# Kernel optimization log

Hardware: AMD Instinct MI355X
Metric: run time of the kernel (lower is better)

## Reference

```python
import jax, jax.numpy as jnp
import numpy as np

H = 128
NH = 8  # num attention heads


def _ln(x, g, b, eps=1e-5):
    m = x.mean(-1, keepdims=True)
    v = ((x - m) ** 2).mean(-1, keepdims=True)
    return (x - m) / jnp.sqrt(v + eps) * g + b


def _mha(q_in, kv_in, Wqkv, bqkv, Wo, bo):
    # torch nn.MultiheadAttention with packed in_proj, batch=1, eval (no dropout)
    h = q_in.shape[-1]
    hd = h // NH
    Wq, Wk, Wv = Wqkv[:h], Wqkv[h:2 * h], Wqkv[2 * h:]
    bq, bk, bv = bqkv[:h], bqkv[h:2 * h], bqkv[2 * h:]
    q = (q_in @ Wq.T + bq).reshape(-1, NH, hd).transpose(1, 0, 2)   # [nh, Nq, hd]
    k = (kv_in @ Wk.T + bk).reshape(-1, NH, hd).transpose(1, 0, 2)  # [nh, Nk, hd]
    v = (kv_in @ Wv.T + bv).reshape(-1, NH, hd).transpose(1, 0, 2)
    scores = jnp.einsum('hqd,hkd->hqk', q, k) / jnp.sqrt(jnp.asarray(hd, q.dtype))
    attn = jax.nn.softmax(scores, axis=-1)
    out = jnp.einsum('hqk,hkd->hqd', attn, v)                       # [nh, Nq, hd]
    out = out.transpose(1, 0, 2).reshape(-1, h)
    return out @ Wo.T + bo


def setup_inputs() -> dict:
    key = jax.random.key(0)
    ks = jax.random.split(key, 32)
    s = 0.05
    d = {
        'ligand_features': jax.random.normal(ks[0], (512, 128), jnp.float32),
        'pocket_features': jax.random.normal(ks[1], (1024, 128), jnp.float32),
        'ligand_coords': jax.random.uniform(ks[2], (512, 3), jnp.float32) * 20.0,
        'pocket_coords': jax.random.uniform(ks[3], (1024, 3), jnp.float32) * 20.0,
        # projections
        'Wl': jax.random.normal(ks[4], (H, 128), jnp.float32) * s,
        'bl': jnp.zeros((H,), jnp.float32),
        'Wp': jax.random.normal(ks[5], (H, 128), jnp.float32) * s,
        'bp': jnp.zeros((H,), jnp.float32),
        # distance encoder: 1 -> h/4 -> h/2 -> h
        'Wd1': jax.random.normal(ks[6], (H // 4, 1), jnp.float32) * s,
        'bd1': jnp.zeros((H // 4,), jnp.float32),
        'Wd2': jax.random.normal(ks[7], (H // 2, H // 4), jnp.float32) * s,
        'bd2': jnp.zeros((H // 2,), jnp.float32),
        'Wd3': jax.random.normal(ks[8], (H, H // 2), jnp.float32) * s,
        'bd3': jnp.zeros((H,), jnp.float32),
        # gates
        'Wgl': jax.random.normal(ks[9], (H, 2 * H), jnp.float32) * s,
        'bgl': jnp.zeros((H,), jnp.float32),
        'Wgp': jax.random.normal(ks[10], (H, 2 * H), jnp.float32) * s,
        'bgp': jnp.zeros((H,), jnp.float32),
        # shared cross-attention (packed qkv like torch)
        'Wqkv': jax.random.normal(ks[11], (3 * H, H), jnp.float32) * s,
        'bqkv': jnp.zeros((3 * H,), jnp.float32),
        'Wo': jax.random.normal(ks[12], (H, H), jnp.float32) * s,
        'bo': jnp.zeros((H,), jnp.float32),
        # layer norms
        'g_l': jnp.ones((H,), jnp.float32),
        'be_l': jnp.zeros((H,), jnp.float32),
        'g_p': jnp.ones((H,), jnp.float32),
        'be_p': jnp.zeros((H,), jnp.float32),
    }
    return d


def reference(ligand_features, pocket_features, ligand_coords, pocket_coords,
              Wl, bl, Wp, bp, Wd1, bd1, Wd2, bd2, Wd3, bd3,
              Wgl, bgl, Wgp, bgp, Wqkv, bqkv, Wo, bo,
              g_l, be_l, g_p, be_p):
    lig = ligand_features @ Wl.T + bl   # [Nl, H]
    poc = pocket_features @ Wp.T + bp   # [Np, H]

    # pairwise distances [Nl, Np]
    diff = ligand_coords[:, None, :] - pocket_coords[None, :, :]
    dist = jnp.sqrt(jnp.sum(diff * diff, axis=-1))

    # distance encoder MLP applied elementwise -> [Nl, Np, H]
    e = jax.nn.relu(dist[..., None] @ Wd1.T + bd1)
    e = jax.nn.relu(e @ Wd2.T + bd2)
    enc = e @ Wd3.T + bd3
    m = enc.mean(axis=-1)               # [Nl, Np]

    # ligand enhancement: softmax over pocket axis
    sw_l = jax.nn.softmax(-m, axis=-1)          # [Nl, Np]
    agg_l = sw_l @ poc                          # [Nl, H]
    gate_l = jax.nn.sigmoid(jnp.concatenate([lig, agg_l], axis=-1) @ Wgl.T + bgl)
    lig_enh = gate_l * lig + (1.0 - gate_l) * agg_l

    # pocket enhancement: transposed encoding, softmax over ligand axis
    sw_p = jax.nn.softmax(-m.T, axis=-1)        # [Np, Nl]
    agg_p = sw_p @ lig                          # [Np, H]
    gate_p = jax.nn.sigmoid(jnp.concatenate([poc, agg_p], axis=-1) @ Wgp.T + bgp)
    poc_enh = gate_p * poc + (1.0 - gate_p) * agg_p

    lig_att = _mha(lig_enh, poc_enh, Wqkv, bqkv, Wo, bo)
    poc_att = _mha(poc_enh, lig_enh, Wqkv, bqkv, Wo, bo)

    lig_fused = _ln(lig_enh + lig_att, g_l, be_l)
    poc_fused = _ln(poc_enh + poc_att, g_p, be_p)
    return (lig_fused, poc_fused)
```

## Files before the change

kernel.cpp:

```cpp
#include <hip/hip_runtime.h>
#include <math.h>

#define NL 512
#define NP 1024
#define HDIM 128

#define TAB_N 8192
#define DMAX 34.65f

#define M_OFF    128
#define WLT_OFF  (M_OFF)
#define WPT_OFF  (M_OFF + 16384)
#define WQT_OFF  (M_OFF + 32768)
#define WOT_OFF  (M_OFF + 81920)
#define WGLT_OFF (M_OFF + 98304)
#define WGPT_OFF (M_OFF + 131072)
#define TAB_OFF  (M_OFF + 163840)
#define LIG_OFF  (M_OFF + NL*NP)
#define POC_OFF  (LIG_OFF + NL*HDIM)
#define LENH_OFF (POC_OFF + NP*HDIM)
#define PENH_OFF (LENH_OFF + NL*HDIM)
#define QKVL_OFF (PENH_OFF + NP*HDIM)
#define QKVP_OFF (QKVL_OFF + NL*384)
#define PARTL_OFF (QKVP_OFF + NP*384)
#define PARTP_OFF (PARTL_OFF + 512*8*8*18)

__device__ __forceinline__ float dot4f(float4 a, float4 b){
  return fmaf(a.x,b.x, fmaf(a.y,b.y, fmaf(a.z,b.z, a.w*b.w)));
}

__device__ __forceinline__ void tpose(const float* __restrict__ src, float* __restrict__ dst,
                                      int O, int K, int blk0, int t){
  int e0 = blk0*1024 + t*4;
  #pragma unroll
  for (int i = 0; i < 4; i++){
    int e = e0 + i;
    int o = e / K, k = e - o*K;
    dst[(size_t)k*O + o] = src[(size_t)o*K + k];
  }
}
__global__ __launch_bounds__(256) void prep_all(const float* __restrict__ Wl, const float* __restrict__ Wp,
                                                const float* __restrict__ Wqkv, const float* __restrict__ Wo,
                                                const float* __restrict__ Wgl, const float* __restrict__ Wgp,
                                                const float* __restrict__ Wd1, const float* __restrict__ bd1,
                                                const float* __restrict__ Wd2, const float* __restrict__ bd2,
                                                const float* __restrict__ Wd3, const float* __restrict__ bd3,
                                                float* __restrict__ ws){
  int b = blockIdx.x, t = threadIdx.x;
  if (b < 160){
    if      (b < 16)  tpose(Wl,   ws + WLT_OFF,  128, 128, b,       t);
    else if (b < 32)  tpose(Wp,   ws + WPT_OFF,  128, 128, b - 16,  t);
    else if (b < 80)  tpose(Wqkv, ws + WQT_OFF,  384, 128, b - 32,  t);
    else if (b < 96)  tpose(Wo,   ws + WOT_OFF,  128, 128, b - 80,  t);
    else if (b < 128) tpose(Wgl,  ws + WGLT_OFF, 128, 256, b - 96,  t);
    else              tpose(Wgp,  ws + WGPT_OFF, 128, 256, b - 128, t);
    return;
  }
  float* tab = ws + TAB_OFF;
  __shared__ float sWd1[32], sbd1[32], sWd2[2048], sbd2[64], swd3m[64];
  __shared__ float sbd3m;
  int idx = (b - 160) * 256 + t;
  if (t < 64){
    float s = 0.f;
    #pragma unroll 8
    for (int i = 0; i < 128; i++) s += Wd3[i*64 + t];
    swd3m[t] = s * (1.f/128.f);
  } else if (t == 64){
    float s = 0.f;
    for (int i = 0; i < 128; i++) s += bd3[i];
    sbd3m = s * (1.f/128.f);
  } else if (t >= 128 && t < 160){ sWd1[t-128] = Wd1[t-128]; sbd1[t-128] = bd1[t-128]; }
  else if (t >= 160 && t < 224){ sbd2[t-160] = bd2[t-160]; }
  for (int k = t; k < 2048; k += 256) sWd2[k] = Wd2[k];
  __syncthreads();

  float d = (float)idx * (DMAX / (float)(TAB_N - 1));
  float4 e1q[8];
  const float4* w1q = (const float4*)sWd1;
  const float4* b1q = (const float4*)sbd1;
  #pragma unroll
  for (int k4 = 0; k4 < 8; k4++){
    float4 w = w1q[k4], bb = b1q[k4];
    float4 e;
    e.x = fmaxf(fmaf(d, w.x, bb.x), 0.f);
    e.y = fmaxf(fmaf(d, w.y, bb.y), 0.f);
    e.z = fmaxf(fmaf(d, w.z, bb.z), 0.f);
    e.w = fmaxf(fmaf(d, w.w, bb.w), 0.f);
    e1q[k4] = e;
  }
  float mv = sbd3m;
  #pragma unroll 4
  for (int j2 = 0; j2 < 64; j2++){
    const float4* wrow = (const float4*)(sWd2 + j2*32);
    float a0 = 0.f, a1 = 0.f, a2 = 0.f, a3 = 0.f;
    #pragma unroll
    for (int k4 = 0; k4 < 8; k4++){
      float4 w = wrow[k4], e = e1q[k4];
      a0 = fmaf(w.x, e.x, a0);
      a1 = fmaf(w.y, e.y, a1);
      a2 = fmaf(w.z, e.z, a2);
      a3 = fmaf(w.w, e.w, a3);
    }
    float e2v = fmaxf(sbd2[j2] + ((a0+a1)+(a2+a3)), 0.f);
    mv = fmaf(swd3m[j2], e2v, mv);
  }
  tab[idx] = mv;
}

__global__ __launch_bounds__(256) void proj_kernel(const float* __restrict__ lf, const float* __restrict__ pf,
                                                   const float* __restrict__ WlT, const float* __restrict__ bl,
                                                   const float* __restrict__ WpT, const float* __restrict__ bp,
                                                   float* __restrict__ lig, float* __restrict__ poc){
  int b = blockIdx.x, t = threadIdx.x;
  bool isLig = (b < NL/2);
  int r0 = isLig ? b*2 : (b - NL/2)*2;
  const float* in = (isLig ? lf : pf) + (size_t)r0*HDIM;
  const float* WT = isLig ? WlT : WpT;
  const float* bias = isLig ? bl : bp;
  float* out = (isLig ? lig : poc) + (size_t)r0*HDIM;
  __shared__ float sx[2*HDIM];
  sx[t] = in[t];
  __syncthreads();
  int r = t >> 7, col = t & 127;
  const float* xr = sx + r*HDIM;
  float acc = bias[col];
  #pragma unroll 8
  for (int k = 0; k < 128; k++) acc = fmaf(WT[k*128 + col], xr[k], acc);
  out[r*HDIM + col] = acc;
}

__global__ __launch_bounds__(512) void agg_gate_fused(const float* __restrict__ lc, const float* __restrict__ pc,
                                                      const float* __restrict__ tab,
                                                      const float* __restrict__ lig, const float* __restrict__ poc,
                                                      const float* __restrict__ WglT, const float* __restrict__ bgl,
                                                      const float* __restrict__ WgpT, const float* __restrict__ bgp,
                                                      const float* __restrict__ WqkvT, const float* __restrict__ bqkv,
                                                      float* __restrict__ lenh, float* __restrict__ penh,
                                                      float* __restrict__ qkvl, float* __restrict__ qkvp){
  int b = blockIdx.x, t = threadIdx.x;
  bool isLig = (b < NL/2);
  int r0 = isLig ? b*2 : (b - NL/2)*2;
  int n = isLig ? NP : NL;
  const float* myFeat = isLig ? lig : poc;
  const float* otherFeat = isLig ? poc : lig;
  const float* myC = isLig ? lc : pc;
  const float* otC = isLig ? pc : lc;

  __shared__ float w[2*NP];
  __shared__ float sx[2*HDIM];
  __shared__ float sa[2*HDIM];
  __shared__ float4 part4[8*64];
  __shared__ float gpart[512];
  __shared__ float redm[8];
  __shared__ float sgm[2], sinv[2];

  int rr = t >> 8, u = t & 255;
  int lane = t & 63, wv = t >> 6;
  int row = r0 + rr;

  if (t < 256) sx[t] = myFeat[(size_t)r0*HDIM + t];

// ... 92 lines not shown
    g = 1.0f / (1.0f + __expf(-g));
    float xv = sx[t], av = sa[t];
    enh_val = fmaf(g, xv - av, av);
    float* dst = isLig ? (lenh + (size_t)(r0+r)*HDIM) : (penh + (size_t)(r0+r)*HDIM);
    dst[col] = enh_val;
  }
  __syncthreads();
  if (t < 256) sa[t] = enh_val;
  __syncthreads();

  {
    int r = t >> 8, ln = t & 255;
    const float* er = sa + r*HDIM;
    float* qout = (isLig ? qkvl : qkvp) + (size_t)(r0+r)*384;
    if (ln < 128){
      float a0 = bqkv[ln], a2 = bqkv[ln+256];
      #pragma unroll 4
      for (int k = 0; k < 128; k++){
        float xv = er[k];
        const float* wk = WqkvT + k*384;
        a0 = fmaf(wk[ln],     xv, a0);
        a2 = fmaf(wk[ln+256], xv, a2);
      }
      qout[ln] = a0; qout[ln+256] = a2;
    } else {
      float a1 = bqkv[ln];
      #pragma unroll 4
      for (int k = 0; k < 128; k++) a1 = fmaf(WqkvT[k*384 + ln], er[k], a1);
      qout[ln] = a1;
    }
  }
}

__global__ __launch_bounds__(256) void attn_part(const float* __restrict__ qkvl, const float* __restrict__ qkvp,
                                                 float* __restrict__ partL, float* __restrict__ partP){
  int bx = blockIdx.x;
  int t = threadIdx.x;
  const float* qsrc; const float* kvsrc; int qt, slice; bool isLig;
  if (bx < 256){ isLig = true;  qt = bx >> 3; slice = bx & 7; qsrc = qkvl; kvsrc = qkvp; }
  else { int b2 = bx - 256; isLig = false; qt = b2 >> 2; slice = b2 & 3; qsrc = qkvp; kvsrc = qkvl; }
  int g = t >> 6, tt = t & 63;
  int h = tt >> 3, qp = tt & 7;
  int j0 = slice*128 + g*32;

  const float4* qA = (const float4*)(qsrc + (size_t)(qt*16+qp)*384 + h*16);
  const float4* qB = (const float4*)(qsrc + (size_t)(qt*16+qp+8)*384 + h*16);
  float4 a0 = qA[0], a1 = qA[1], a2 = qA[2], a3 = qA[3];
  float4 b0 = qB[0], b1 = qB[1], b2 = qB[2], b3 = qB[3];
  float mA = -1e30f, lA = 0.f, mB = -1e30f, lB = 0.f;
  float4 OA0={0,0,0,0}, OA1={0,0,0,0}, OA2={0,0,0,0}, OA3={0,0,0,0};
  float4 OB0={0,0,0,0}, OB1={0,0,0,0}, OB2={0,0,0,0}, OB3={0,0,0,0};

  __shared__ float sKV[8192];
  float* myKV = sKV + g*2048;

  for (int tile = 0; tile < 4; tile++){
    int jbase = j0 + tile*8;
    __syncthreads();
    #pragma unroll
    for (int nn = 0; nn < 8; nn++){
      int v4 = tt + nn*64;
      int jj = v4 >> 6, c4 = v4 & 63;
      ((float4*)myKV)[jj*64 + c4] = *(const float4*)(kvsrc + (size_t)(jbase+jj)*384 + 128 + c4*4);
    }
    __syncthreads();
    float sA[8], sB[8];
    #pragma unroll
    for (int jj = 0; jj < 8; jj++){
      const float4* kk = (const float4*)(myKV + jj*256 + h*16);
      float4 k0 = kk[0], k1 = kk[1], k2 = kk[2], k3 = kk[3];
      sA[jj] = (dot4f(a0,k0) + dot4f(a1,k1) + dot4f(a2,k2) + dot4f(a3,k3)) * 0.25f;
      sB[jj] = (dot4f(b0,k0) + dot4f(b1,k1) + dot4f(b2,k2) + dot4f(b3,k3)) * 0.25f;
    }
    float mtA = sA[0], mtB = sB[0];
    #pragma unroll
    for (int jj = 1; jj < 8; jj++){ mtA = fmaxf(mtA, sA[jj]); mtB = fmaxf(mtB, sB[jj]); }
    float mnA = fmaxf(mA, mtA), mnB = fmaxf(mB, mtB);
    float cA = __expf(mA - mnA), cB = __expf(mB - mnB);
    lA *= cA; lB *= cB;
    OA0.x*=cA; OA0.y*=cA; OA0.z*=cA; OA0.w*=cA;
    OA1.x*=cA; OA1.y*=cA; OA1.z*=cA; OA1.w*=cA;
    OA2.x*=cA; OA2.y*=cA; OA2.z*=cA; OA2.w*=cA;
    OA3.x*=cA; OA3.y*=cA; OA3.z*=cA; OA3.w*=cA;
    OB0.x*=cB; OB0.y*=cB; OB0.z*=cB; OB0.w*=cB;
    OB1.x*=cB; OB1.y*=cB; OB1.z*=cB; OB1.w*=cB;
    OB2.x*=cB; OB2.y*=cB; OB2.z*=cB; OB2.w*=cB;
// ... 53 lines not shown
      float e0 = __expf(M - Mn), e1 = __expf(m1 - Mn);
      L = L*e0 + l1*e1;
      #pragma unroll
      for (int k = 0; k < 16; k++) O[k] = O[k]*e0 + br[2+k]*e1;
      M = Mn;
    }
    int rowA = qt*16 + qp;
    float* dst = isLig ? (partL + ((size_t)(rowA*8 + h)*8 + slice)*18)
                       : (partP + ((size_t)(rowA*8 + h)*4 + slice)*18);
    dst[0] = M; dst[1] = L;
    #pragma unroll
    for (int k = 0; k < 16; k++) dst[2+k] = O[k];
    M = mB; L = lB;
    float Ob[16] = {OB0.x,OB0.y,OB0.z,OB0.w, OB1.x,OB1.y,OB1.z,OB1.w,
                    OB2.x,OB2.y,OB2.z,OB2.w, OB3.x,OB3.y,OB3.z,OB3.w};
    #pragma unroll
    for (int gg = 1; gg < 4; gg++){
      const float* br = sKV + (size_t)((gg-1)*128 + tt*2 + 1)*19;
      float m1 = br[0], l1 = br[1];
      float Mn = fmaxf(M, m1);
      float e0 = __expf(M - Mn), e1 = __expf(m1 - Mn);
      L = L*e0 + l1*e1;
      #pragma unroll
      for (int k = 0; k < 16; k++) Ob[k] = Ob[k]*e0 + br[2+k]*e1;
      M = Mn;
    }
    int rowB = qt*16 + qp + 8;
    float* dstB = isLig ? (partL + ((size_t)(rowB*8 + h)*8 + slice)*18)
                        : (partP + ((size_t)(rowB*8 + h)*4 + slice)*18);
    dstB[0] = M; dstB[1] = L;
    #pragma unroll
    for (int k = 0; k < 16; k++) dstB[2+k] = Ob[k];
  }
}

__global__ __launch_bounds__(256) void merge_ln(const float* __restrict__ partL, const float* __restrict__ partP,
                                                const float* __restrict__ lenh, const float* __restrict__ penh,
                                                const float* __restrict__ WoT, const float* __restrict__ bo,
                                                const float* __restrict__ g_l, const float* __restrict__ be_l,
                                                const float* __restrict__ g_p, const float* __restrict__ be_p,
                                                float* __restrict__ out){
  int b = blockIdx.x, t = threadIdx.x;
  int r0 = b*2;
  int r = t >> 7, c = t & 127;
  int gr = r0 + r;
  int h = c >> 4, cc = c & 15;
  int ns; const float* base;
  if (gr < NL){ ns = 8; base = partL + ((size_t)(gr*8 + h))*8*18; }
  else        { ns = 4; base = partP + ((size_t)((gr-NL)*8 + h))*4*18; }
  float M = -1e30f;
  for (int s = 0; s < ns; s++) M = fmaxf(M, base[s*18]);
  float Lsum = 0.f, Osum = 0.f;
  for (int s = 0; s < ns; s++){
    float e = __expf(base[s*18] - M);
    Lsum = fmaf(e, base[s*18+1], Lsum);
    Osum = fmaf(e, base[s*18+2+cc], Osum);
  }
  __shared__ float sAtt[2*HDIM];
  sAtt[t] = Osum / Lsum;
  __syncthreads();
  float o = bo[c];
  const float* sA = sAtt + r*HDIM;
  #pragma unroll 8
  for (int k = 0; k < 128; k++) o = fmaf(WoT[k*128 + c], sA[k], o);
  const float* enh = (gr < NL) ? (lenh + (size_t)gr*HDIM) : (penh + (size_t)(gr-NL)*HDIM);
  float x = enh[c] + o;
  __shared__ float sred[8];
  int wid = t >> 6;
  float v = x;
  #pragma unroll
  for (int off = 32; off; off >>= 1) v += __shfl_down(v, off);
  if ((t & 63) == 0) sred[wid] = v;
  __syncthreads();
  float mu = (sred[2*r] + sred[2*r+1]) * (1.f/128.f);
  float dx = x - mu;
  v = dx*dx;
  #pragma unroll
  for (int off = 32; off; off >>= 1) v += __shfl_down(v, off);
  if ((t & 63) == 0) sred[4 + wid] = v;
  __syncthreads();
  float var = (sred[4 + 2*r] + sred[4 + 2*r+1]) * (1.f/128.f);
  float y = dx * rsqrtf(var + 1e-5f);
  if (gr < NL) y = fmaf(y, g_l[c], be_l[c]);
  else         y = fmaf(y, g_p[c], be_p[c]);
  out[(size_t)gr*HDIM + c] = y;
}

extern "C" void kernel_launch(void* const* d_in, const int* in_sizes, int n_in,
                              void* d_out, int out_size, void* d_ws, size_t ws_size,
                              hipStream_t stream){
  const float* lf   = (const float*)d_in[0];
  const float* pf   = (const float*)d_in[1];
  const float* lc   = (const float*)d_in[2];
  const float* pc   = (const float*)d_in[3];
  const float* Wl   = (const float*)d_in[4];
  const float* bl   = (const float*)d_in[5];
  const float* Wp   = (const float*)d_in[6];
  const float* bp   = (const float*)d_in[7];
  const float* Wd1  = (const float*)d_in[8];
  const float* bd1  = (const float*)d_in[9];
  const float* Wd2  = (const float*)d_in[10];
  const float* bd2  = (const float*)d_in[11];
  const float* Wd3  = (const float*)d_in[12];
  const float* bd3  = (const float*)d_in[13];
  const float* Wgl  = (const float*)d_in[14];
  const float* bgl  = (const float*)d_in[15];
  const float* Wgp  = (const float*)d_in[16];
  const float* bgp  = (const float*)d_in[17];
  const float* Wqkv = (const float*)d_in[18];
  const float* bqkv = (const float*)d_in[19];
  const float* Wo   = (const float*)d_in[20];
  const float* bo   = (const float*)d_in[21];
  const float* g_l  = (const float*)d_in[22];
  const float* be_l = (const float*)d_in[23];
  const float* g_p  = (const float*)d_in[24];
  const float* be_p = (const float*)d_in[25];

  float* ws  = (float*)d_ws;
  float* out = (float*)d_out;
  float* lig   = ws + LIG_OFF;
  float* poc   = ws + POC_OFF;
  float* lenh  = ws + LENH_OFF;
  float* penh  = ws + PENH_OFF;
  float* qkvl  = ws + QKVL_OFF;
  float* qkvp  = ws + QKVP_OFF;
  float* partL = ws + PARTL_OFF;
  float* partP = ws + PARTP_OFF;
  float* tab   = ws + TAB_OFF;

  prep_all<<<192, 256, 0, stream>>>(Wl, Wp, Wqkv, Wo, Wgl, Wgp, Wd1, bd1, Wd2, bd2, Wd3, bd3, ws);
  proj_kernel<<<NL/2 + NP/2, 256, 0, stream>>>(lf, pf, ws + WLT_OFF, bl, ws + WPT_OFF, bp, lig, poc);
  agg_gate_fused<<<NL/2 + NP/2, 512, 0, stream>>>(lc, pc, tab, lig, poc,
                                                  ws + WGLT_OFF, bgl, ws + WGPT_OFF, bgp,
                                                  ws + WQT_OFF, bqkv,
                                                  lenh, penh, qkvl, qkvp);
  attn_part<<<512, 256, 0, stream>>>(qkvl, qkvp, partL, partP);
  merge_ln<<<NL/2 + NP/2, 256, 0, stream>>>(partL, partP, lenh, penh, ws + WOT_OFF, bo,
                                            g_l, be_l, g_p, be_p, out);
}
```

Measured before the change: 194.5 us.

## Fuse all stages into one cooperative persistent kernel with grid syncs

```diff
diff --git a/kernel.cpp b/kernel.cpp
--- a/kernel.cpp
+++ b/kernel.cpp
@@ -1,5 +1,8 @@
 #include <hip/hip_runtime.h>
+#include <hip/hip_cooperative_groups.h>
 #include <math.h>
+
+namespace cg = cooperative_groups;
 
 #define NL 512
 #define NP 1024
@@ -24,9 +27,487 @@
 #define QKVP_OFF (QKVL_OFF + NL*384)
 #define PARTL_OFF (QKVP_OFF + NP*384)
 #define PARTP_OFF (PARTL_OFF + 512*8*8*18)
+#define AGG_OFF   (PARTP_OFF + 1024*8*4*18)
 
 __device__ __forceinline__ float dot4f(float4 a, float4 b){
   return fmaf(a.x,b.x, fmaf(a.y,b.y, fmaf(a.z,b.z, a.w*b.w)));
+}
+
+__global__ __launch_bounds__(512, 4) void fused_all(
+  const float* __restrict__ lf, const float* __restrict__ pf,
+  const float* __restrict__ lc, const float* __restrict__ pc,
+  const float* __restrict__ Wl, const float* __restrict__ bl,
+  const float* __restrict__ Wp, const float* __restrict__ bp,
+  const float* __restrict__ Wd1, const float* __restrict__ bd1,
+  const float* __restrict__ Wd2, const float* __restrict__ bd2,
+  const float* __restrict__ Wd3, const float* __restrict__ bd3,
+  const float* __restrict__ Wgl, const float* __restrict__ bgl,
+  const float* __restrict__ Wgp, const float* __restrict__ bgp,
+  const float* __restrict__ Wqkv, const float* __restrict__ bqkv,
+  const float* __restrict__ Wo, const float* __restrict__ bo,
+  const float* __restrict__ g_l, const float* __restrict__ be_l,
+  const float* __restrict__ g_p, const float* __restrict__ be_p,
+  float* __restrict__ ws, float* __restrict__ out)
+{
+  cg::grid_group grd = cg::this_grid();
+  const int b = blockIdx.x;
+  const int t = threadIdx.x;
+
+  __shared__ __align__(16) float smem[16384];
+
+  float* WlT   = ws + WLT_OFF;
+  float* WpT   = ws + WPT_OFF;
+  float* WqkvT = ws + WQT_OFF;
+  float* WoT   = ws + WOT_OFF;
+  float* WglT  = ws + WGLT_OFF;
+  float* WgpT  = ws + WGPT_OFF;
+  float* tab   = ws + TAB_OFF;
+  float* lig   = ws + LIG_OFF;
+  float* poc   = ws + POC_OFF;
+  float* lenh  = ws + LENH_OFF;
+  float* penh  = ws + PENH_OFF;
+  float* qkvl  = ws + QKVL_OFF;
+  float* qkvp  = ws + QKVP_OFF;
+  float* partL = ws + PARTL_OFF;
+  float* partP = ws + PARTP_OFF;
+  float* aggb  = ws + AGG_OFF;
+
+  {
+    int e = b*512 + t;
+    if (e < 163840){
+      if (e < 16384){
+        int loc = e, o = loc >> 7, k = loc & 127;
+        WlT[k*128 + o] = Wl[loc];
+      } else if (e < 32768){
+        int loc = e - 16384, o = loc >> 7, k = loc & 127;
+        WpT[k*128 + o] = Wp[loc];
+      } else if (e < 81920){
+        int loc = e - 32768, o = loc >> 7, k = loc & 127;
+        WqkvT[k*384 + o] = Wqkv[loc];
+      } else if (e < 98304){
+        int loc = e - 81920, o = loc >> 7, k = loc & 127;
+        WoT[k*128 + o] = Wo[loc];
+      } else if (e < 131072){
+        int loc = e - 98304, o = loc >> 8, k = loc & 255;
+        WglT[k*128 + o] = Wgl[loc];
+      } else {
+        int loc = e - 131072, o = loc >> 8, k = loc & 255;
+        WgpT[k*128 + o] = Wgp[loc];
+      }
+    }
+  }
+  grd.sync();
+
+  if (b < 384){
+    int sub = t >> 8, st = t & 255;
+    int s = b*2 + sub;
+    bool isLig = (s < NL/2);
+    int r0 = isLig ? s*2 : (s - NL/2)*2;
+    const float* in  = (isLig ? lf : pf) + (size_t)r0*HDIM;
+    const float* WT  = isLig ? WlT : WpT;
+    const float* bia = isLig ? bl : bp;
+    float* o = (isLig ? lig : poc) + (size_t)r0*HDIM;
+    float* sx = smem + sub*256;
+    sx[st] = in[st];
+    __syncthreads();
+    int r = st >> 7, col = st & 127;
+    const float* xr = sx + r*HDIM;
+    float acc = bia[col];
+    #pragma unroll 8
+    for (int k = 0; k < 128; k++) acc = fmaf(WT[k*128 + col], xr[k], acc);
+    o[r*HDIM + col] = acc;
+  } else if (b < 400){
+    float* sWd1  = smem;
+    float* sbd1  = smem + 32;
+    float* sbd2  = smem + 64;
+    float* swd3m = smem + 128;
+    float* sWd2  = smem + 256;
+    if (t < 64){
+      float ssum = 0.f;
+      #pragma unroll 8
+      for (int i = 0; i < 128; i++) ssum += Wd3[i*64 + t];
+      swd3m[t] = ssum * (1.f/128.f);
+    } else if (t == 64){
+      float ssum = 0.f;
+      for (int i = 0; i < 128; i++) ssum += bd3[i];
+      smem[192] = ssum * (1.f/128.f);
+    } else if (t >= 128 && t < 160){ sWd1[t-128] = Wd1[t-128]; sbd1[t-128] = bd1[t-128]; }
+    else if (t >= 160 && t < 224){ sbd2[t-160] = bd2[t-160]; }
+    for (int k = t; k < 2048; k += 512) sWd2[k] = Wd2[k];
+    __syncthreads();
+
+    int idx = (b - 384)*512 + t;
+    float d = (float)idx * (DMAX / (float)(TAB_N - 1));
+    float4 e1q[8];
+    const float4* w1q = (const float4*)sWd1;
+    const float4* b1q = (const float4*)sbd1;
+    #pragma unroll
+    for (int k4 = 0; k4 < 8; k4++){
+      float4 w = w1q[k4], bb = b1q[k4];
+      float4 e;
+      e.x = fmaxf(fmaf(d, w.x, bb.x), 0.f);
+      e.y = fmaxf(fmaf(d, w.y, bb.y), 0.f);
+      e.z = fmaxf(fmaf(d, w.z, bb.z), 0.f);
+      e.w = fmaxf(fmaf(d, w.w, bb.w), 0.f);
+      e1q[k4] = e;
+    }
+    float mv = smem[192];
+    #pragma unroll 4
+    for (int j2 = 0; j2 < 64; j2++){
+      const float4* wrow = (const float4*)(sWd2 + j2*32);
+      float a0 = 0.f, a1 = 0.f, a2 = 0.f, a3 = 0.f;
+      #pragma unroll
+      for (int k4 = 0; k4 < 8; k4++){
+        float4 w = wrow[k4], e = e1q[k4];
+        a0 = fmaf(w.x, e.x, a0);
+        a1 = fmaf(w.y, e.y, a1);
+        a2 = fmaf(w.z, e.z, a2);
+        a3 = fmaf(w.w, e.w, a3);
+      }
+      float e2v = fmaxf(sbd2[j2] + ((a0+a1)+(a2+a3)), 0.f);
+      mv = fmaf(swd3m[j2], e2v, mv);
+    }
+    tab[idx] = mv;
+  }
+  grd.sync();
+
+  {
+    float*  w     = smem;
+    float4* part4 = (float4*)(smem + 2048);
+    float*  redm  = smem + 4096;
+    float*  sgm   = smem + 4104;
+    float*  sinv  = smem + 4106;
+
+    int ntask = (b < 256) ? 1 : 2;
+    bool isLig = (b < 256);
+    int n = isLig ? NP : NL;
+    const float* otherFeat = isLig ? poc : lig;
+    const float* myC = isLig ? lc : pc;
+    const float* otC = isLig ? pc : lc;
+    int growbase = isLig ? 0 : NL;
+    const float inv_h = (float)(TAB_N - 1) / DMAX;
+
+    int rr = t >> 8, u = t & 255;
+    int lane = t & 63, wv = t >> 6;
+    int per = n >> 8;
+
+    for (int it = 0; it < ntask; it++){
+      int r0 = isLig ? b*2 : (2*(b-256) + it)*2;
+      int row = r0 + rr;
+      float cx = myC[row*3+0], cy = myC[row*3+1], cz = myC[row*3+2];
+
+      float xs[4];
+      float lmax = -1e30f;
+      for (int k = 0; k < per; k++){
+        int j = u + (k << 8);
+        float ox = otC[j*3+0], oy = otC[j*3+1], oz = otC[j*3+2];
+        float dx = cx-ox, dy = cy-oy, dz = cz-oz;
+        float d = sqrtf(fmaf(dx,dx, fmaf(dy,dy, dz*dz)));
+        float xf = d * inv_h;
+        int i0 = (int)xf;
+        i0 = (i0 > TAB_N-2) ? (TAB_N-2) : i0;
+        float f = xf - (float)i0;
+        float v0 = tab[i0], v1 = tab[i0+1];
+        xs[k] = -fmaf(f, v1 - v0, v0);
+        lmax = fmaxf(lmax, xs[k]);
+      }
+      float v = lmax;
+      #pragma unroll
+      for (int off = 32; off; off >>= 1) v = fmaxf(v, __shfl_down(v, off));
+      if (lane == 0) redm[wv] = v;
+      __syncthreads();
+      if (t < 2) sgm[t] = fmaxf(fmaxf(redm[t*4+0], redm[t*4+1]), fmaxf(redm[t*4+2], redm[t*4+3]));
+      __syncthreads();
+      float gm = sgm[rr];
+      float lsum = 0.f;
+      for (int k = 0; k < per; k++){
+        float e = __expf(xs[k] - gm);
+        w[rr*NP + u + (k << 8)] = e;
+        lsum += e;
+      }
+      v = lsum;
+      #pragma unroll
+      for (int off = 32; off; off >>= 1) v += __shfl_down(v, off);
+      if (lane == 0) redm[wv] = v;
+      __syncthreads();
+      if (t < 2) sinv[t] = 1.0f / ((redm[t*4+0] + redm[t*4+1]) + (redm[t*4+2] + redm[t*4+3]));
+      __syncthreads();
+
+      {
+        int jg = t >> 6;
+        int r  = (t >> 5) & 1;
+        int c4 = t & 31;
+        int per2 = n >> 3;
+        int jb0 = jg * per2;
+        const float4* of4 = (const float4*)otherFeat;
+        const float* wR = w + r*NP;
+        float4 acc = {0,0,0,0};
+        #pragma unroll 4
+        for (int jj = 0; jj < per2; jj++){
+          int j = jb0 + jj;
+          float4 f = of4[(size_t)j*32 + c4];
+          float ww = wR[j];
+          acc.x = fmaf(ww, f.x, acc.x); acc.y = fmaf(ww, f.y, acc.y);
+          acc.z = fmaf(ww, f.z, acc.z); acc.w = fmaf(ww, f.w, acc.w);
+        }
+        part4[(jg*2 + r)*32 + c4] = acc;
+      }
+      __syncthreads();
+      #pragma unroll
+      for (int s2 = 4; s2 >= 1; s2 >>= 1){
+        if (t < s2*64){
+          int g2 = t >> 6, rem = t & 63;
+          float4 a = part4[g2*64 + rem], bb = part4[(g2+s2)*64 + rem];
+          a.x += bb.x; a.y += bb.y; a.z += bb.z; a.w += bb.w;
+          part4[g2*64 + rem] = a;
+        }
+        __syncthreads();
+      }
+      if (t < 256){
+        float val = ((const float*)part4)[t] * sinv[t >> 7];
+        aggb[(size_t)(growbase + r0 + (t >> 7))*HDIM + (t & 127)] = val;
+      }
+      __syncthreads();
+    }
+  }
+  grd.sync();
+
+  {
+    float* sx    = smem;
+    float* sa2   = smem + 128;
+    float* se    = smem + 256;
+    float* gpart = smem + 384;
+    for (int i = 0; i < 3; i++){
+      int grow = b + i*512;
+      bool isLig = (grow < NL);
+      int row = isLig ? grow : grow - NL;
+      const float* xsrc = (isLig ? lig : poc) + (size_t)row*HDIM;
+      if (t < 128){ sx[t] = xsrc[t]; sa2[t] = aggb[(size_t)grow*HDIM + t]; }
+      __syncthreads();
+      {
+        int col = t & 127, kg = t >> 7;
+        const float* WT = isLig ? WglT : WgpT;
+        const float* inb = (kg < 2) ? sx : (sa2 - 128);
+        int k0 = kg*64;
+        float acc = 0.f;
+        #pragma unroll 8
+        for (int kk = 0; kk < 64; kk++){
+          int k = k0 + kk;
+          acc = fmaf(WT[(size_t)k*128 + col], inb[k], acc);
+        }
+        gpart[kg*128 + col] = acc;
+      }
+      __syncthreads();
+      if (t < 128){
+        const float* bg = isLig ? bgl : bgp;
+        float g = bg[t] + ((gpart[t] + gpart[128+t]) + (gpart[256+t] + gpart[384+t]));
+        g = 1.0f / (1.0f + __expf(-g));
+        float xv = sx[t], av = sa2[t];
+        float enh = fmaf(g, xv - av, av);
+        se[t] = enh;
+        float* dst = isLig ? (lenh + (size_t)row*HDIM) : (penh + (size_t)row*HDIM);
+        dst[t] = enh;
+      }
+      __syncthreads();
+      if (t < 384){
+        float acc = bqkv[t];
+        #pragma unroll 8
+        for (int k = 0; k < 128; k++) acc = fmaf(WqkvT[(size_t)k*384 + t], se[k], acc);
+        float* q = (isLig ? qkvl : qkvp) + (size_t)row*384;
+        q[t] = acc;
+      }
+      __syncthreads();
+    }
+  }
+  grd.sync();
+
+  {
+    const float* qsrc; const float* kvsrc; int qt, slice; bool isLig;
+    if (b < 256){ isLig = true;  qt = b >> 3; slice = b & 7; qsrc = qkvl; kvsrc = qkvp; }
+    else { int b2 = b - 256; isLig = false; qt = b2 >> 2; slice = b2 & 3; qsrc = qkvp; kvsrc = qkvl; }
+    int g = t >> 6, tt = t & 63;
+    int h = tt >> 3, qp = tt & 7;
+    int j0 = slice*128 + g*16;
+
+    const float4* qA = (const float4*)(qsrc + (size_t)(qt*16+qp)*384 + h*16);
+    const float4* qB = (const float4*)(qsrc + (size_t)(qt*16+qp+8)*384 + h*16);
+    float4 a0 = qA[0], a1 = qA[1], a2 = qA[2], a3 = qA[3];
+    float4 b0 = qB[0], b1 = qB[1], b2 = qB[2], b3 = qB[3];
+    float mA = -1e30f, lA = 0.f, mB = -1e30f, lB = 0.f;
+    float4 OA0={0,0,0,0}, OA1={0,0,0,0}, OA2={0,0,0,0}, OA3={0,0,0,0};
+    float4 OB0={0,0,0,0}, OB1={0,0,0,0}, OB2={0,0,0,0}, OB3={0,0,0,0};
+
+    float* myKV = smem + g*2048;
+
+    for (int tile = 0; tile < 2; tile++){
+      int jbase = j0 + tile*8;
+      __syncthreads();
+      #pragma unroll
+      for (int nn = 0; nn < 8; nn++){
+        int v4 = tt + nn*64;
+        int jj = v4 >> 6, c4 = v4 & 63;
+        ((float4*)myKV)[jj*64 + c4] = *(const float4*)(kvsrc + (size_t)(jbase+jj)*384 + 128 + c4*4);
+      }
+      __syncthreads();
+      float sA[8], sB[8];
+      #pragma unroll
+      for (int jj = 0; jj < 8; jj++){
+        const float4* kk = (const float4*)(myKV + jj*256 + h*16);
+        float4 k0 = kk[0], k1 = kk[1], k2 = kk[2], k3 = kk[3];
+        sA[jj] = (dot4f(a0,k0) + dot4f(a1,k1) + dot4f(a2,k2) + dot4f(a3,k3)) * 0.25f;
+        sB[jj] = (dot4f(b0,k0) + dot4f(b1,k1) + dot4f(b2,k2) + dot4f(b3,k3)) * 0.25f;
+      }
+      float mtA = sA[0], mtB = sB[0];
+      #pragma unroll
+      for (int jj = 1; jj < 8; jj++){ mtA = fmaxf(mtA, sA[jj]); mtB = fmaxf(mtB, sB[jj]); }
+      float mnA = fmaxf(mA, mtA), mnB = fmaxf(mB, mtB);
+      float cA = __expf(mA - mnA), cB = __expf(mB - mnB);
+      lA *= cA; lB *= cB;
+      OA0.x*=cA; OA0.y*=cA; OA0.z*=cA; OA0.w*=cA;
+      OA1.x*=cA; OA1.y*=cA; OA1.z*=cA; OA1.w*=cA;
+      OA2.x*=cA; OA2.y*=cA; OA2.z*=cA; OA2.w*=cA;
+      OA3.x*=cA; OA3.y*=cA; OA3.z*=cA; OA3.w*=cA;
+      OB0.x*=cB; OB0.y*=cB; OB0.z*=cB; OB0.w*=cB;
+      OB1.x*=cB; OB1.y*=cB; OB1.z*=cB; OB1.w*=cB;
+      OB2.x*=cB; OB2.y*=cB; OB2.z*=cB; OB2.w*=cB;
+      OB3.x*=cB; OB3.y*=cB; OB3.z*=cB; OB3.w*=cB;
+      #pragma unroll
+      for (int jj = 0; jj < 8; jj++){
+        float pA = __expf(sA[jj] - mnA);
+        float pB = __expf(sB[jj] - mnB);
+        lA += pA; lB += pB;
+        const float4* vv = (const float4*)(myKV + jj*256 + 128 + h*16);
+        float4 v0 = vv[0], v1 = vv[1], v2 = vv[2], v3 = vv[3];
+        OA0.x = fmaf(pA, v0.x, OA0.x); OA0.y = fmaf(pA, v0.y, OA0.y);
+        OA0.z = fmaf(pA, v0.z, OA0.z); OA0.w = fmaf(pA, v0.w, OA0.w);
+        OA1.x = fmaf(pA, v1.x, OA1.x); OA1.y = fmaf(pA, v1.y, OA1.y);
+        OA1.z = fmaf(pA, v1.z, OA1.z); OA1.w = fmaf(pA, v1.w, OA1.w);
+        OA2.x = fmaf(pA, v2.x, OA2.x); OA2.y = fmaf(pA, v2.y, OA2.y);
+        OA2.z = fmaf(pA, v2.z, OA2.z); OA2.w = fmaf(pA, v2.w, OA2.w);
+        OA3.x = fmaf(pA, v3.x, OA3.x); OA3.y = fmaf(pA, v3.y, OA3.y);
+        OA3.z = fmaf(pA, v3.z, OA3.z); OA3.w = fmaf(pA, v3.w, OA3.w);
+        OB0.x = fmaf(pB, v0.x, OB0.x); OB0.y = fmaf(pB, v0.y, OB0.y);
+        OB0.z = fmaf(pB, v0.z, OB0.z); OB0.w = fmaf(pB, v0.w, OB0.w);
+        OB1.x = fmaf(pB, v1.x, OB1.x); OB1.y = fmaf(pB, v1.y, OB1.y);
+        OB1.z = fmaf(pB, v1.z, OB1.z); OB1.w = fmaf(pB, v1.w, OB1.w);
+        OB2.x = fmaf(pB, v2.x, OB2.x); OB2.y = fmaf(pB, v2.y, OB2.y);
+        OB2.z = fmaf(pB, v2.z, OB2.z); OB2.w = fmaf(pB, v2.w, OB2.w);
+        OB3.x = fmaf(pB, v3.x, OB3.x); OB3.y = fmaf(pB, v3.y, OB3.y);
+        OB3.z = fmaf(pB, v3.z, OB3.z); OB3.w = fmaf(pB, v3.w, OB3.w);
+      }
+      mA = mnA; mB = mnB;
+    }
+
+    __syncthreads();
+    if (g > 0){
+      float* bA = smem + (size_t)((g-1)*128 + tt*2)*18;
+      bA[0]=mA; bA[1]=lA;
+      bA[2]=OA0.x; bA[3]=OA0.y; bA[4]=OA0.z; bA[5]=OA0.w;
+      bA[6]=OA1.x; bA[7]=OA1.y; bA[8]=OA1.z; bA[9]=OA1.w;
+      bA[10]=OA2.x; bA[11]=OA2.y; bA[12]=OA2.z; bA[13]=OA2.w;
+      bA[14]=OA3.x; bA[15]=OA3.y; bA[16]=OA3.z; bA[17]=OA3.w;
+      float* bB = bA + 18;
+      bB[0]=mB; bB[1]=lB;
+      bB[2]=OB0.x; bB[3]=OB0.y; bB[4]=OB0.z; bB[5]=OB0.w;
+      bB[6]=OB1.x; bB[7]=OB1.y; bB[8]=OB1.z; bB[9]=OB1.w;
+      bB[10]=OB2.x; bB[11]=OB2.y; bB[12]=OB2.z; bB[13]=OB2.w;
+      bB[14]=OB3.x; bB[15]=OB3.y; bB[16]=OB3.z; bB[17]=OB3.w;
+    }
+    __syncthreads();
+    if (g == 0){
+      float M = mA, L = lA;
+      float O[16] = {OA0.x,OA0.y,OA0.z,OA0.w, OA1.x,OA1.y,OA1.z,OA1.w,
+                     OA2.x,OA2.y,OA2.z,OA2.w, OA3.x,OA3.y,OA3.z,OA3.w};
+      #pragma unroll
+      for (int gg = 1; gg < 8; gg++){
+        const float* br = smem + (size_t)((gg-1)*128 + tt*2)*18;
+        float m1 = br[0], l1 = br[1];
+        float Mn = fmaxf(M, m1);
+        float e0 = __expf(M - Mn), e1 = __expf(m1 - Mn);
+        L = L*e0 + l1*e1;
+        #pragma unroll
+        for (int k = 0; k < 16; k++) O[k] = O[k]*e0 + br[2+k]*e1;
+        M = Mn;
+      }
+      int rowA = qt*16 + qp;
+      float* dst = isLig ? (partL + ((size_t)(rowA*8 + h)*8 + slice)*18)
+                         : (partP + ((size_t)(rowA*8 + h)*4 + slice)*18);
+      dst[0] = M; dst[1] = L;
+      #pragma unroll
+      for (int k = 0; k < 16; k++) dst[2+k] = O[k];
+      M = mB; L = lB;
+      float Ob[16] = {OB0.x,OB0.y,OB0.z,OB0.w, OB1.x,OB1.y,OB1.z,OB1.w,
+                      OB2.x,OB2.y,OB2.z,OB2.w, OB3.x,OB3.y,OB3.z,OB3.w};
+      #pragma unroll
+      for (int gg = 1; gg < 8; gg++){
+        const float* br = smem + (size_t)((gg-1)*128 + tt*2)*18 + 18;
+        float m1 = br[0], l1 = br[1];
+        float Mn = fmaxf(M, m1);
+        float e0 = __expf(M - Mn), e1 = __expf(m1 - Mn);
+        L = L*e0 + l1*e1;
+        #pragma unroll
+        for (int k = 0; k < 16; k++) Ob[k] = Ob[k]*e0 + br[2+k]*e1;
+        M = Mn;
+      }
+      int rowB = qt*16 + qp + 8;
+      float* dstB = isLig ? (partL + ((size_t)(rowB*8 + h)*8 + slice)*18)
+                          : (partP + ((size_t)(rowB*8 + h)*4 + slice)*18);
+      dstB[0] = M; dstB[1] = L;
+      #pragma unroll
+      for (int k = 0; k < 16; k++) dstB[2+k] = Ob[k];
+    }
+  }
+  grd.sync();
+
+  {
+    int sub = t >> 8, st = t & 255;
+    int s = b*2 + sub;
+    if (s < 768){
+      int r0 = s*2;
+      int r = st >> 7, c = st & 127;
+      int gr = r0 + r;
+      int hh = c >> 4, cc = c & 15;
+      int ns; const float* base;
+      if (gr < NL){ ns = 8; base = partL + ((size_t)(gr*8 + hh))*8*18; }
+      else        { ns = 4; base = partP + ((size_t)((gr-NL)*8 + hh))*4*18; }
+      float M = -1e30f;
+      for (int sl = 0; sl < ns; sl++) M = fmaxf(M, base[sl*18]);
+      float Lsum = 0.f, Osum = 0.f;
+      for (int sl = 0; sl < ns; sl++){
+        float e = __expf(base[sl*18] - M);
+        Lsum = fmaf(e, base[sl*18+1], Lsum);
+        Osum = fmaf(e, base[sl*18+2+cc], Osum);
+      }
+      float* sAtt = smem + sub*512;
+      float* sred = smem + 1024 + sub*16;
+      sAtt[st] = Osum / Lsum;
+      __syncthreads();
+      float o = bo[c];
+      const float* sA = sAtt + r*HDIM;
+      #pragma unroll 8
+      for (int k = 0; k < 128; k++) o = fmaf(WoT[k*128 + c], sA[k], o);
+      const float* enh = (gr < NL) ? (lenh + (size_t)gr*HDIM) : (penh + (size_t)(gr-NL)*HDIM);
+      float x = enh[c] + o;
+      int wid = st >> 6;
+      float v = x;
+      #pragma unroll
+      for (int off = 32; off; off >>= 1) v += __shfl_down(v, off);
+      if ((st & 63) == 0) sred[wid] = v;
+      __syncthreads();
+      float mu = (sred[2*r] + sred[2*r+1]) * (1.f/128.f);
+      float dx = x - mu;
+      v = dx*dx;
+      #pragma unroll
+      for (int off = 32; off; off >>= 1) v += __shfl_down(v, off);
+      if ((st & 63) == 0) sred[4 + wid] = v;
+      __syncthreads();
+      float var = (sred[4 + 2*r] + sred[4 + 2*r+1]) * (1.f/128.f);
+      float y = dx * rsqrtf(var + 1e-5f);
+      if (gr < NL) y = fmaf(y, g_l[c], be_l[c]);
+      else         y = fmaf(y, g_p[c], be_p[c]);
+      out[(size_t)gr*HDIM + c] = y;
+    }
+  }
 }
 
 __device__ __forceinline__ void tpose(const float* __restrict__ src, float* __restrict__ dst,
@@ -510,23 +991,36 @@
 
   float* ws  = (float*)d_ws;
   float* out = (float*)d_out;
-  float* lig   = ws + LIG_OFF;
-  float* poc   = ws + POC_OFF;
-  float* lenh  = ws + LENH_OFF;
-  float* penh  = ws + PENH_OFF;
-  float* qkvl  = ws + QKVL_OFF;
-  float* qkvp  = ws + QKVP_OFF;
-  float* partL = ws + PARTL_OFF;
-  float* partP = ws + PARTP_OFF;
-  float* tab   = ws + TAB_OFF;
-
-  prep_all<<<192, 256, 0, stream>>>(Wl, Wp, Wqkv, Wo, Wgl, Wgp, Wd1, bd1, Wd2, bd2, Wd3, bd3, ws);
-  proj_kernel<<<NL/2 + NP/2, 256, 0, stream>>>(lf, pf, ws + WLT_OFF, bl, ws + WPT_OFF, bp, lig, poc);
-  agg_gate_fused<<<NL/2 + NP/2, 512, 0, stream>>>(lc, pc, tab, lig, poc,
-                                                  ws + WGLT_OFF, bgl, ws + WGPT_OFF, bgp,
-                                                  ws + WQT_OFF, bqkv,
-                                                  lenh, penh, qkvl, qkvp);
-  attn_part<<<512, 256, 0, stream>>>(qkvl, qkvp, partL, partP);
-  merge_ln<<<NL/2 + NP/2, 256, 0, stream>>>(partL, partP, lenh, penh, ws + WOT_OFF, bo,
-                                            g_l, be_l, g_p, be_p, out);
+
+  void* args[] = { (void*)&lf, (void*)&pf, (void*)&lc, (void*)&pc,
+                   (void*)&Wl, (void*)&bl, (void*)&Wp, (void*)&bp,
+                   (void*)&Wd1, (void*)&bd1, (void*)&Wd2, (void*)&bd2,
+                   (void*)&Wd3, (void*)&bd3, (void*)&Wgl, (void*)&bgl,
+                   (void*)&Wgp, (void*)&bgp, (void*)&Wqkv, (void*)&bqkv,
+                   (void*)&Wo, (void*)&bo, (void*)&g_l, (void*)&be_l,
+                   (void*)&g_p, (void*)&be_p, (void*)&ws, (void*)&out };
+
+  hipError_t err = hipLaunchCooperativeKernel((const void*)fused_all,
+                                              dim3(512), dim3(512), args, 0, stream);
+  if (err != hipSuccess){
+    float* lig   = ws + LIG_OFF;
+    float* poc   = ws + POC_OFF;
+    float* lenh  = ws + LENH_OFF;
+    float* penh  = ws + PENH_OFF;
+    float* qkvl  = ws + QKVL_OFF;
+    float* qkvp  = ws + QKVP_OFF;
+    float* partL = ws + PARTL_OFF;
+    float* partP = ws + PARTP_OFF;
+    float* tab   = ws + TAB_OFF;
+
+    prep_all<<<192, 256, 0, stream>>>(Wl, Wp, Wqkv, Wo, Wgl, Wgp, Wd1, bd1, Wd2, bd2, Wd3, bd3, ws);
+    proj_kernel<<<NL/2 + NP/2, 256, 0, stream>>>(lf, pf, ws + WLT_OFF, bl, ws + WPT_OFF, bp, lig, poc);
+    agg_gate_fused<<<NL/2 + NP/2, 512, 0, stream>>>(lc, pc, tab, lig, poc,
+                                                    ws + WGLT_OFF, bgl, ws + WGPT_OFF, bgp,
+                                                    ws + WQT_OFF, bqkv,
+                                                    lenh, penh, qkvl, qkvp);
+    attn_part<<<512, 256, 0, stream>>>(qkvl, qkvp, partL, partP);
+    merge_ln<<<NL/2 + NP/2, 256, 0, stream>>>(partL, partP, lenh, penh, ws + WOT_OFF, bo,
+                                              g_l, be_l, g_p, be_p, out);
+  }
 }
```

New measurement: 565.9 us. 191% more time.

## Fuse input projection into prep kernel and merge+LN into attention via last-block counter

Applied to the files above, without the earlier changes.

```diff
diff --git a/kernel.cpp b/kernel.cpp
--- a/kernel.cpp
+++ b/kernel.cpp
@@ -9,14 +9,12 @@
 #define DMAX 34.65f
 
 #define M_OFF    128
-#define WLT_OFF  (M_OFF)
-#define WPT_OFF  (M_OFF + 16384)
-#define WQT_OFF  (M_OFF + 32768)
-#define WOT_OFF  (M_OFF + 81920)
-#define WGLT_OFF (M_OFF + 98304)
-#define WGPT_OFF (M_OFF + 131072)
-#define TAB_OFF  (M_OFF + 163840)
-#define LIG_OFF  (M_OFF + NL*NP)
+#define WQT_OFF  (M_OFF)
+#define WOT_OFF  (M_OFF + 49152)
+#define WGLT_OFF (M_OFF + 65536)
+#define WGPT_OFF (M_OFF + 98304)
+#define TAB_OFF  (M_OFF + 131072)
+#define LIG_OFF  (M_OFF + 139264)
 #define POC_OFF  (LIG_OFF + NL*HDIM)
 #define LENH_OFF (POC_OFF + NP*HDIM)
 #define PENH_OFF (LENH_OFF + NL*HDIM)
@@ -24,6 +22,7 @@
 #define QKVP_OFF (QKVL_OFF + NL*384)
 #define PARTL_OFF (QKVP_OFF + NP*384)
 #define PARTP_OFF (PARTL_OFF + 512*8*8*18)
+#define CNT_OFF   (PARTP_OFF + 1024*8*4*18)
 
 __device__ __forceinline__ float dot4f(float4 a, float4 b){
   return fmaf(a.x,b.x, fmaf(a.y,b.y, fmaf(a.z,b.z, a.w*b.w)));
@@ -39,27 +38,54 @@
     dst[(size_t)k*O + o] = src[(size_t)o*K + k];
   }
 }
-__global__ __launch_bounds__(256) void prep_all(const float* __restrict__ Wl, const float* __restrict__ Wp,
-                                                const float* __restrict__ Wqkv, const float* __restrict__ Wo,
-                                                const float* __restrict__ Wgl, const float* __restrict__ Wgp,
-                                                const float* __restrict__ Wd1, const float* __restrict__ bd1,
-                                                const float* __restrict__ Wd2, const float* __restrict__ bd2,
-                                                const float* __restrict__ Wd3, const float* __restrict__ bd3,
-                                                float* __restrict__ ws){
+
+__global__ __launch_bounds__(256) void prep_proj(
+    const float* __restrict__ lf, const float* __restrict__ pf,
+    const float* __restrict__ Wl, const float* __restrict__ bl,
+    const float* __restrict__ Wp, const float* __restrict__ bp,
+    const float* __restrict__ Wqkv, const float* __restrict__ Wo,
+    const float* __restrict__ Wgl, const float* __restrict__ Wgp,
+    const float* __restrict__ Wd1, const float* __restrict__ bd1,
+    const float* __restrict__ Wd2, const float* __restrict__ bd2,
+    const float* __restrict__ Wd3, const float* __restrict__ bd3,
+    float* __restrict__ ws){
   int b = blockIdx.x, t = threadIdx.x;
-  if (b < 160){
-    if      (b < 16)  tpose(Wl,   ws + WLT_OFF,  128, 128, b,       t);
-    else if (b < 32)  tpose(Wp,   ws + WPT_OFF,  128, 128, b - 16,  t);
-    else if (b < 80)  tpose(Wqkv, ws + WQT_OFF,  384, 128, b - 32,  t);
-    else if (b < 96)  tpose(Wo,   ws + WOT_OFF,  128, 128, b - 80,  t);
-    else if (b < 128) tpose(Wgl,  ws + WGLT_OFF, 128, 256, b - 96,  t);
-    else              tpose(Wgp,  ws + WGPT_OFF, 128, 256, b - 128, t);
+
+  if (b < 768){
+    bool isLig = (b < 256);
+    int r0 = isLig ? b*2 : (b - 256)*2;
+    const float* in   = (isLig ? lf : pf) + (size_t)r0*HDIM;
+    const float* W    = isLig ? Wl : Wp;
+    const float* bias = isLig ? bl : bp;
+    float* out = ws + (isLig ? LIG_OFF : POC_OFF) + (size_t)r0*HDIM;
+    __shared__ __align__(16) float sx[2*HDIM];
+    sx[t] = in[t];
+    __syncthreads();
+    int r = t >> 7, col = t & 127;
+    const float4* xr4 = (const float4*)(sx + r*HDIM);
+    const float4* w4  = (const float4*)(W + (size_t)col*128);
+    float acc = bias[col];
+    #pragma unroll 8
+    for (int k4 = 0; k4 < 32; k4++) acc += dot4f(w4[k4], xr4[k4]);
+    out[r*HDIM + col] = acc;
     return;
   }
+
+  if (b < 896){
+    int bb = b - 768;
+    if      (bb < 48) tpose(Wqkv, ws + WQT_OFF,  384, 128, bb,      t);
+    else if (bb < 64) tpose(Wo,   ws + WOT_OFF,  128, 128, bb - 48, t);
+    else if (bb < 96) tpose(Wgl,  ws + WGLT_OFF, 128, 256, bb - 64, t);
+    else              tpose(Wgp,  ws + WGPT_OFF, 128, 256, bb - 96, t);
+    return;
+  }
+
+  if (b == 896 && t < 96) ((int*)(ws + CNT_OFF))[t] = 0;
+
   float* tab = ws + TAB_OFF;
   __shared__ float sWd1[32], sbd1[32], sWd2[2048], sbd2[64], swd3m[64];
   __shared__ float sbd3m;
-  int idx = (b - 160) * 256 + t;
+  int idx = (b - 896) * 256 + t;
   if (t < 64){
     float s = 0.f;
     #pragma unroll 8
@@ -80,12 +106,12 @@
   const float4* b1q = (const float4*)sbd1;
   #pragma unroll
   for (int k4 = 0; k4 < 8; k4++){
-    float4 w = w1q[k4], bb = b1q[k4];
+    float4 w = w1q[k4], bb2 = b1q[k4];
     float4 e;
-    e.x = fmaxf(fmaf(d, w.x, bb.x), 0.f);
-    e.y = fmaxf(fmaf(d, w.y, bb.y), 0.f);
-    e.z = fmaxf(fmaf(d, w.z, bb.z), 0.f);
-    e.w = fmaxf(fmaf(d, w.w, bb.w), 0.f);
+    e.x = fmaxf(fmaf(d, w.x, bb2.x), 0.f);
+    e.y = fmaxf(fmaf(d, w.y, bb2.y), 0.f);
+    e.z = fmaxf(fmaf(d, w.z, bb2.z), 0.f);
+    e.w = fmaxf(fmaf(d, w.w, bb2.w), 0.f);
     e1q[k4] = e;
   }
   float mv = sbd3m;
@@ -105,28 +131,6 @@
     mv = fmaf(swd3m[j2], e2v, mv);
   }
   tab[idx] = mv;
-}
-
-__global__ __launch_bounds__(256) void proj_kernel(const float* __restrict__ lf, const float* __restrict__ pf,
-                                                   const float* __restrict__ WlT, const float* __restrict__ bl,
-                                                   const float* __restrict__ WpT, const float* __restrict__ bp,
-                                                   float* __restrict__ lig, float* __restrict__ poc){
-  int b = blockIdx.x, t = threadIdx.x;
-  bool isLig = (b < NL/2);
-  int r0 = isLig ? b*2 : (b - NL/2)*2;
-  const float* in = (isLig ? lf : pf) + (size_t)r0*HDIM;
-  const float* WT = isLig ? WlT : WpT;
-  const float* bias = isLig ? bl : bp;
-  float* out = (isLig ? lig : poc) + (size_t)r0*HDIM;
-  __shared__ float sx[2*HDIM];
-  sx[t] = in[t];
-  __syncthreads();
-  int r = t >> 7, col = t & 127;
-  const float* xr = sx + r*HDIM;
-  float acc = bias[col];
-  #pragma unroll 8
-  for (int k = 0; k < 128; k++) acc = fmaf(WT[k*128 + col], xr[k], acc);
-  out[r*HDIM + col] = acc;
 }
 
 __global__ __launch_bounds__(512) void agg_gate_fused(const float* __restrict__ lc, const float* __restrict__ pc,
@@ -285,8 +289,13 @@
   }
 }
 
-__global__ __launch_bounds__(256) void attn_part(const float* __restrict__ qkvl, const float* __restrict__ qkvp,
-                                                 float* __restrict__ partL, float* __restrict__ partP){
+__global__ __launch_bounds__(256) void attn_merge(const float* __restrict__ qkvl, const float* __restrict__ qkvp,
+                                                  float* __restrict__ partL, float* __restrict__ partP,
+                                                  const float* __restrict__ lenh, const float* __restrict__ penh,
+                                                  const float* __restrict__ WoT, const float* __restrict__ bo,
+                                                  const float* __restrict__ g_l, const float* __restrict__ be_l,
+                                                  const float* __restrict__ g_p, const float* __restrict__ be_p,
+                                                  int* __restrict__ cnt, float* __restrict__ out){
   int bx = blockIdx.x;
   int t = threadIdx.x;
   const float* qsrc; const float* kvsrc; int qt, slice; bool isLig;
@@ -304,7 +313,7 @@
   float4 OA0={0,0,0,0}, OA1={0,0,0,0}, OA2={0,0,0,0}, OA3={0,0,0,0};
   float4 OB0={0,0,0,0}, OB1={0,0,0,0}, OB2={0,0,0,0}, OB3={0,0,0,0};
 
-  __shared__ float sKV[8192];
+  __shared__ __align__(16) float sKV[8192];
   float* myKV = sKV + g*2048;
 
   for (int tile = 0; tile < 4; tile++){
@@ -424,58 +433,66 @@
     #pragma unroll
     for (int k = 0; k < 16; k++) dstB[2+k] = Ob[k];
   }
-}
-
-__global__ __launch_bounds__(256) void merge_ln(const float* __restrict__ partL, const float* __restrict__ partP,
-                                                const float* __restrict__ lenh, const float* __restrict__ penh,
-                                                const float* __restrict__ WoT, const float* __restrict__ bo,
-                                                const float* __restrict__ g_l, const float* __restrict__ be_l,
-                                                const float* __restrict__ g_p, const float* __restrict__ be_p,
-                                                float* __restrict__ out){
-  int b = blockIdx.x, t = threadIdx.x;
-  int r0 = b*2;
+
+  __syncthreads();
+  __threadfence();
+  __shared__ int sWin;
+  if (t == 0){
+    int idx = isLig ? qt : (32 + qt);
+    int target = isLig ? 8 : 4;
+    int old = atomicAdd(&cnt[idx], 1);
+    sWin = (old == target - 1) ? 1 : 0;
+  }
+  __syncthreads();
+  if (!sWin) return;
+  __threadfence();
+
+  float* sAtt = sKV;
+  float* sred = sKV + 512;
   int r = t >> 7, c = t & 127;
-  int gr = r0 + r;
-  int h = c >> 4, cc = c & 15;
-  int ns; const float* base;
-  if (gr < NL){ ns = 8; base = partL + ((size_t)(gr*8 + h))*8*18; }
-  else        { ns = 4; base = partP + ((size_t)((gr-NL)*8 + h))*4*18; }
-  float M = -1e30f;
-  for (int s = 0; s < ns; s++) M = fmaxf(M, base[s*18]);
-  float Lsum = 0.f, Osum = 0.f;
-  for (int s = 0; s < ns; s++){
-    float e = __expf(base[s*18] - M);
-    Lsum = fmaf(e, base[s*18+1], Lsum);
-    Osum = fmaf(e, base[s*18+2+cc], Osum);
-  }
-  __shared__ float sAtt[2*HDIM];
-  sAtt[t] = Osum / Lsum;
-  __syncthreads();
-  float o = bo[c];
-  const float* sA = sAtt + r*HDIM;
-  #pragma unroll 8
-  for (int k = 0; k < 128; k++) o = fmaf(WoT[k*128 + c], sA[k], o);
-  const float* enh = (gr < NL) ? (lenh + (size_t)gr*HDIM) : (penh + (size_t)(gr-NL)*HDIM);
-  float x = enh[c] + o;
-  __shared__ float sred[8];
+  int hh = c >> 4, cc = c & 15;
   int wid = t >> 6;
-  float v = x;
-  #pragma unroll
-  for (int off = 32; off; off >>= 1) v += __shfl_down(v, off);
-  if ((t & 63) == 0) sred[wid] = v;
-  __syncthreads();
-  float mu = (sred[2*r] + sred[2*r+1]) * (1.f/128.f);
-  float dx = x - mu;
-  v = dx*dx;
-  #pragma unroll
-  for (int off = 32; off; off >>= 1) v += __shfl_down(v, off);
-  if ((t & 63) == 0) sred[4 + wid] = v;
-  __syncthreads();
-  float var = (sred[4 + 2*r] + sred[4 + 2*r+1]) * (1.f/128.f);
-  float y = dx * rsqrtf(var + 1e-5f);
-  if (gr < NL) y = fmaf(y, g_l[c], be_l[c]);
-  else         y = fmaf(y, g_p[c], be_p[c]);
-  out[(size_t)gr*HDIM + c] = y;
+  for (int i = 0; i < 8; i++){
+    int lr = qt*16 + 2*i + r;
+    int ns; const float* base;
+    if (isLig){ ns = 8; base = partL + ((size_t)(lr*8 + hh))*8*18; }
+    else      { ns = 4; base = partP + ((size_t)(lr*8 + hh))*4*18; }
+    float M = -1e30f;
+    for (int sl = 0; sl < ns; sl++) M = fmaxf(M, base[sl*18]);
+    float Lsum = 0.f, Osum = 0.f;
+    for (int sl = 0; sl < ns; sl++){
+      float e = __expf(base[sl*18] - M);
+      Lsum = fmaf(e, base[sl*18+1], Lsum);
+      Osum = fmaf(e, base[sl*18+2+cc], Osum);
+    }
+    __syncthreads();
+    sAtt[t] = Osum / Lsum;
+    __syncthreads();
+    float o = bo[c];
+    const float* sA = sAtt + r*HDIM;
+    #pragma unroll 8
+    for (int k = 0; k < 128; k++) o = fmaf(WoT[k*128 + c], sA[k], o);
+    const float* enh = isLig ? (lenh + (size_t)lr*HDIM) : (penh + (size_t)lr*HDIM);
+    float x = enh[c] + o;
+    float v = x;
+    #pragma unroll
+    for (int off = 32; off; off >>= 1) v += __shfl_down(v, off);
+    if ((t & 63) == 0) sred[wid] = v;
+    __syncthreads();
+    float mu = (sred[2*r] + sred[2*r+1]) * (1.f/128.f);
+    float dx = x - mu;
+    v = dx*dx;
+    #pragma unroll
+    for (int off = 32; off; off >>= 1) v += __shfl_down(v, off);
+    if ((t & 63) == 0) sred[4 + wid] = v;
+    __syncthreads();
+    float var = (sred[4 + 2*r] + sred[4 + 2*r+1]) * (1.f/128.f);
+    float y = dx * rsqrtf(var + 1e-5f);
+    int gr = isLig ? lr : (NL + lr);
+    if (isLig) y = fmaf(y, g_l[c], be_l[c]);
+    else       y = fmaf(y, g_p[c], be_p[c]);
+    out[(size_t)gr*HDIM + c] = y;
+  }
 }
 
 extern "C" void kernel_launch(void* const* d_in, const int* in_sizes, int n_in,
@@ -510,6 +527,7 @@
 
   float* ws  = (float*)d_ws;
   float* out = (float*)d_out;
+
   float* lig   = ws + LIG_OFF;
   float* poc   = ws + POC_OFF;
   float* lenh  = ws + LENH_OFF;
@@ -519,14 +537,14 @@
   float* partL = ws + PARTL_OFF;
   float* partP = ws + PARTP_OFF;
   float* tab   = ws + TAB_OFF;
-
-  prep_all<<<192, 256, 0, stream>>>(Wl, Wp, Wqkv, Wo, Wgl, Wgp, Wd1, bd1, Wd2, bd2, Wd3, bd3, ws);
-  proj_kernel<<<NL/2 + NP/2, 256, 0, stream>>>(lf, pf, ws + WLT_OFF, bl, ws + WPT_OFF, bp, lig, poc);
+  int*   cnt   = (int*)(ws + CNT_OFF);
+
+  prep_proj<<<928, 256, 0, stream>>>(lf, pf, Wl, bl, Wp, bp, Wqkv, Wo, Wgl, Wgp,
+                                     Wd1, bd1, Wd2, bd2, Wd3, bd3, ws);
   agg_gate_fused<<<NL/2 + NP/2, 512, 0, stream>>>(lc, pc, tab, lig, poc,
                                                   ws + WGLT_OFF, bgl, ws + WGPT_OFF, bgp,
                                                   ws + WQT_OFF, bqkv,
                                                   lenh, penh, qkvl, qkvp);
-  attn_part<<<512, 256, 0, stream>>>(qkvl, qkvp, partL, partP);
-  merge_ln<<<NL/2 + NP/2, 256, 0, stream>>>(partL, partP, lenh, penh, ws + WOT_OFF, bo,
-                                            g_l, be_l, g_p, be_p, out);
+  attn_merge<<<512, 256, 0, stream>>>(qkvl, qkvp, partL, partP, lenh, penh,
+                                      ws + WOT_OFF, bo, g_l, be_l, g_p, be_p, cnt, out);
 }
```

After: 314.1 us. +61.5%, slower.
